# Kernel tuning notes

Hardware: AMD Instinct MI355X
Metric: run time of the kernel (lower is better)

Reference implementation:

```python
import jax, jax.numpy as jnp
import numpy as np

DIM_K = 128
MODEL_DIM = 1024
B, S = 8, 2048

def setup_inputs() -> dict:
    key = jax.random.key(0)
    k1, k2, k3, k4, k5, k6, k7 = jax.random.split(key, 7)
    return {
        "query": jax.random.normal(k1, (B, S, MODEL_DIM), dtype=jnp.float32),
        "key": jax.random.normal(k2, (B, S, MODEL_DIM), dtype=jnp.float32),
        "value": jax.random.normal(k3, (B, S, MODEL_DIM), dtype=jnp.float32),
        "mask": jax.random.randint(k4, (B, S, S), 0, 2, dtype=jnp.int32),
        # nn.Linear(model_dim, dim_k, bias=False): weight shape [dim_k, model_dim]
        "Wq": jax.random.normal(k5, (DIM_K, MODEL_DIM), dtype=jnp.float32) * (MODEL_DIM ** -0.5),
        "Wk": jax.random.normal(k6, (DIM_K, MODEL_DIM), dtype=jnp.float32) * (MODEL_DIM ** -0.5),
        "Wv": jax.random.normal(k7, (DIM_K, MODEL_DIM), dtype=jnp.float32) * (MODEL_DIM ** -0.5),
    }

def reference(query, key, value, mask, Wq, Wk, Wv):
    # projections: y = x @ W.T
    q = jnp.einsum('bsm,km->bsk', query, Wq)
    k = jnp.einsum('bsm,km->bsk', key, Wk)
    v = jnp.einsum('bsm,km->bsk', value, Wv)
    scale = 1.0 / jnp.sqrt(jnp.float32(DIM_K))
    pre_score = jnp.einsum('bqk,bsk->bqs', q, k) * scale  # [B,Sq,Sk]
    pre_score = jnp.where(mask == 0, jnp.float32(-1e9), pre_score)
    score = jax.nn.softmax(pre_score, axis=-1)
    return jnp.einsum('bqs,bsk->bqk', score, v)
```

## Files before the change

kernel.cpp:

```cpp
#include <hip/hip_runtime.h>
#include <hip/hip_fp16.h>

#define SEQ 2048
#define DMODEL 1024
#define DK 128

typedef _Float16 f16x8 __attribute__((ext_vector_type(8)));
typedef float    f32x4 __attribute__((ext_vector_type(4)));

#define L2E 1.44269504088896340736f

#define WS_Q  393216
#define WS_K  2490368
#define WS_VT 4587520
#define WS_F16_BYTES 13369344ull

__global__ __launch_bounds__(256) void wconv_kernel(
    const float* __restrict__ wq, const float* __restrict__ wk,
    const float* __restrict__ wv, _Float16* __restrict__ w16)
{
    int i = blockIdx.x * 256 + threadIdx.x;
    int p = i >> 17;
    int j = i & 131071;
    const float* src = (p == 0) ? wq : ((p == 1) ? wk : wv);
    float f = src[j];
    if (p == 0) f *= 0.08838834764831845f;
    w16[i] = (_Float16)f;
}

__global__ __launch_bounds__(256, 3) void proj_kernel(
    const float* __restrict__ xq, const float* __restrict__ xk,
    const float* __restrict__ xv, const _Float16* __restrict__ w16,
    _Float16* __restrict__ qws, _Float16* __restrict__ kws, _Float16* __restrict__ vtws)
{
    const int p = blockIdx.y;
    const float* __restrict__ x = (p == 0) ? xq : ((p == 1) ? xk : xv);
    const _Float16* __restrict__ w = w16 + p * 131072;

    const int mtile = blockIdx.x;
    const int m0 = mtile << 6;
    const int t = threadIdx.x;
    const int wv_ = t >> 6;
    const int lane = t & 63;
    const int l15 = lane & 15, g = lane >> 4;
    const int mw = m0 + wv_ * 16;

    __shared__ __align__(16) _Float16 smem[18432];

    f32x4 acc[8];
#pragma unroll
    for (int nt = 0; nt < 8; ++nt) acc[nt] = (f32x4){0.f, 0.f, 0.f, 0.f};

    const float* x0 = x + (size_t)(mw + l15) * 1024 + g * 8;
    const int srow = t >> 3, skc = t & 7;
    const _Float16* wsrc = w + (size_t)srow * 1024 + skc * 8;
    const int sdst = srow * 72 + skc * 8;

    f16x8 wreg[2][4];
    f32x4 areg[2][4];

#pragma unroll
    for (int j = 0; j < 4; ++j)
        wreg[0][j] = *(const f16x8*)(wsrc + (size_t)j * 32 * 1024);
#pragma unroll
    for (int s = 0; s < 2; ++s) {
        areg[0][s * 2]     = *(const f32x4*)(x0 + s * 32);
        areg[0][s * 2 + 1] = *(const f32x4*)(x0 + s * 32 + 4);
    }

#pragma unroll
    for (int kt = 0; kt < 16; ++kt) {
        const int c = kt & 1;
        _Float16* buf = smem + c * 9216;

#pragma unroll
        for (int j = 0; j < 4; ++j)
            *(f16x8*)(buf + j * 32 * 72 + sdst) = wreg[c][j];
        __syncthreads();

        if (kt < 15) {
#pragma unroll
            for (int j = 0; j < 4; ++j)
                wreg[c ^ 1][j] = *(const f16x8*)(wsrc + (size_t)j * 32 * 1024
                                                 + (kt + 1) * 64);
#pragma unroll
            for (int s = 0; s < 2; ++s) {
                areg[c ^ 1][s * 2]     = *(const f32x4*)(x0 + (kt + 1) * 64 + s * 32);
                areg[c ^ 1][s * 2 + 1] = *(const f32x4*)(x0 + (kt + 1) * 64 + s * 32 + 4);
            }
        }

#pragma unroll
        for (int s = 0; s < 2; ++s) {
            f16x8 af;
#pragma unroll
            for (int j = 0; j < 4; ++j) {
                af[j]     = (_Float16)areg[c][s * 2][j];
                af[4 + j] = (_Float16)areg[c][s * 2 + 1][j];
            }
#pragma unroll
            for (int nt = 0; nt < 8; ++nt) {
                f16x8 bf = *(const f16x8*)(buf + (nt * 16 + l15) * 72 + s * 32 + g * 8);
                acc[nt] = __builtin_amdgcn_mfma_f32_16x16x32_f16(af, bf, acc[nt], 0, 0, 0);
            }
        }
    }

    __syncthreads();
    _Float16* olds = smem;
#pragma unroll
    for (int nt = 0; nt < 8; ++nt)
#pragma unroll
        for (int r = 0; r < 4; ++r) {
            int rowl = wv_ * 16 + g * 4 + r;
            int col = nt * 16 + l15;
            _Float16 v = (_Float16)acc[nt][r];
            if (p < 2) olds[rowl * 136 + col] = v;
            else       olds[col * 72 + rowl] = v;
        }
    __syncthreads();

    if (p < 2) {
#pragma unroll
        for (int i = 0; i < 4; ++i) {
            int idx = i * 256 + t;
            int row = idx >> 4, ck = idx & 15;
            f16x8 v = *(const f16x8*)(olds + row * 136 + ck * 8);
            _Float16* dst = ((p == 0) ? qws : kws) + (size_t)(m0 + row) * 128 + ck * 8;
            *(f16x8*)dst = v;
        }
    } else {
        const int bq = mtile >> 5, s0 = (mtile & 31) << 6;
#pragma unroll
        for (int i = 0; i < 4; ++i) {
            int idx = i * 256 + t;
            int row = idx >> 3, ck = idx & 7;
            f16x8 v = *(const f16x8*)(olds + row * 72 + ck * 8);
            _Float16* dst = vtws + ((size_t)(bq * 128 + row)) * 2048 + s0 + ck * 8;
            *(f16x8*)dst = v;
        }
    }
}

__global__ __launch_bounds__(256) void flash_kernel(
    const _Float16* __restrict__ qws, const _Float16* __restrict__ kws,
    const _Float16* __restrict__ vtws, const int* __restrict__ mask,
    float* __restrict__ out, float* __restrict__ part, float* __restrict__ mlbuf,
    int ktp)
{
    const int bb = blockIdx.x & 7;
    const int rest = blockIdx.x >> 3;
    const int mtile = rest & 31;
    const int jsplit = rest >> 5;
    const int sq0 = mtile << 6;
    const int t = threadIdx.x;
    const int wv_ = t >> 6;
    const int lane = t & 63;
    const int l15 = lane & 15, g = lane >> 4;

    __shared__ __align__(16) _Float16 smem[22528];
    _Float16* klds = smem;
    _Float16* vtlds = smem + 8704;
    _Float16* plds = smem + 17920 + wv_ * 1152;

    f16x8 qf[4];
    {
        const _Float16* qp = qws + ((size_t)(bb * 2048 + sq0 + wv_ * 16 + l15)) * 128 + g * 8;
#pragma unroll
        for (int ks = 0; ks < 4; ++ks) qf[ks] = *(const f16x8*)(qp + ks * 32);
    }

    f32x4 o[8];
#pragma unroll
    for (int nt = 0; nt < 8; ++nt) o[nt] = (f32x4){0.f, 0.f, 0.f, 0.f};
    float m_run[4], l_run[4];
#pragma unroll
    for (int r = 0; r < 4; ++r) { m_run[r] = -__builtin_inff(); l_run[r] = 0.f; }

    const int* mbase = mask + ((size_t)(bb * 2048 + sq0 + wv_ * 16 + g * 4)) * 2048 + l15;

    const int kt_begin = jsplit * ktp, kt_end = kt_begin + ktp;
    for (int kt = kt_begin; kt < kt_end; ++kt) {
        const int n0 = kt << 6;
        __syncthreads();
#pragma unroll
        for (int i = 0; i < 8; ++i) {
            int idx = i * 256 + t;
            if (idx < 1024) {
                int row = idx >> 4, ck = idx & 15;
                *(f16x8*)(klds + row * 136 + ck * 8) =
                    *(const f16x8*)(kws + ((size_t)(bb * 2048 + n0 + row)) * 128 + ck * 8);
            } else {
                int v = idx - 1024;
                int row = v >> 3, ck = v & 7;
                *(f16x8*)(vtlds + row * 72 + ck * 8) =
                    *(const f16x8*)(vtws + ((size_t)(bb * 128 + row)) * 2048 + n0 + ck * 8);
            }
        }
        __syncthreads();

        int mv[4][4];
#pragma unroll
        for (int nt = 0; nt < 4; ++nt)
#pragma unroll
            for (int r = 0; r < 4; ++r)
                mv[nt][r] = mbase[(size_t)r * 2048 + n0 + nt * 16];

        f32x4 sf[4];
#pragma unroll
        for (int nt = 0; nt < 4; ++nt) sf[nt] = (f32x4){0.f, 0.f, 0.f, 0.f};
#pragma unroll
        for (int nt = 0; nt < 4; ++nt) {
            const _Float16* kp = klds + (nt * 16 + l15) * 136 + g * 8;
#pragma unroll
            for (int ks = 0; ks < 4; ++ks) {
                f16x8 bfk = *(const f16x8*)(kp + ks * 32);
                sf[nt] = __builtin_amdgcn_mfma_f32_16x16x32_f16(qf[ks], bfk, sf[nt], 0, 0, 0);
            }
        }

        float mx[4], mnew[4], alpha[4], psum[4];
#pragma unroll
        for (int r = 0; r < 4; ++r)
            mx[r] = fmaxf(fmaxf(sf[0][r], sf[1][r]), fmaxf(sf[2][r], sf[3][r]));
#pragma unroll
        for (int off = 1; off < 16; off <<= 1)
#pragma unroll
            for (int r = 0; r < 4; ++r)
                mx[r] = fmaxf(mx[r], __shfl_xor(mx[r], off, 64));
#pragma unroll
        for (int r = 0; r < 4; ++r) {
            mnew[r] = fmaxf(m_run[r], mx[r]);
            alpha[r] = exp2f((m_run[r] - mnew[r]) * L2E);
            psum[r] = 0.f;
        }
#pragma unroll
        for (int nt = 0; nt < 4; ++nt)
#pragma unroll
            for (int r = 0; r < 4; ++r) {
                float pv = exp2f((sf[nt][r] - mnew[r]) * L2E);
                pv = mv[nt][r] ? pv : 0.f;
                psum[r] += pv;
                plds[(g * 4 + r) * 72 + nt * 16 + l15] = (_Float16)pv;
            }
#pragma unroll
        for (int off = 1; off < 16; off <<= 1)
#pragma unroll
            for (int r = 0; r < 4; ++r)
                psum[r] += __shfl_xor(psum[r], off, 64);
#pragma unroll
        for (int r = 0; r < 4; ++r) {
            l_run[r] = l_run[r] * alpha[r] + psum[r];
            m_run[r] = mnew[r];
        }
#pragma unroll
        for (int nt = 0; nt < 8; ++nt)
#pragma unroll
            for (int r = 0; r < 4; ++r) o[nt][r] *= alpha[r];

        f16x8 pa[2];
#pragma unroll
        for (int ks2 = 0; ks2 < 2; ++ks2)
            pa[ks2] = *(const f16x8*)(plds + l15 * 72 + ks2 * 32 + g * 8);

#pragma unroll
        for (int nt2 = 0; nt2 < 8; ++nt2) {
            const _Float16* vp = vtlds + (nt2 * 16 + l15) * 72 + g * 8;
#pragma unroll
            for (int ks2 = 0; ks2 < 2; ++ks2) {
                f16x8 bfv = *(const f16x8*)(vp + ks2 * 32);
                o[nt2] = __builtin_amdgcn_mfma_f32_16x16x32_f16(pa[ks2], bfv, o[nt2], 0, 0, 0);
            }
        }
    }

    if (part == nullptr) {
        float inv[4];
#pragma unroll
        for (int r = 0; r < 4; ++r) inv[r] = 1.0f / l_run[r];
#pragma unroll
        for (int nt2 = 0; nt2 < 8; ++nt2)
#pragma unroll
            for (int r = 0; r < 4; ++r)
                out[((size_t)(bb * 2048 + sq0 + wv_ * 16 + g * 4 + r)) * 128 + nt2 * 16 + l15] =
                    o[nt2][r] * inv[r];
    } else {
#pragma unroll
        for (int nt2 = 0; nt2 < 8; ++nt2)
#pragma unroll
            for (int r = 0; r < 4; ++r) {
                size_t rowg = (size_t)(bb * 2048 + sq0 + wv_ * 16 + g * 4 + r);
                part[((size_t)jsplit * 16384 + rowg) * 128 + nt2 * 16 + l15] = o[nt2][r];
            }
        if (l15 == 0) {
#pragma unroll
            for (int r = 0; r < 4; ++r) {
                size_t rowg = (size_t)(bb * 2048 + sq0 + wv_ * 16 + g * 4 + r);
                mlbuf[((size_t)jsplit * 16384 + rowg) * 2]     = m_run[r];
                mlbuf[((size_t)jsplit * 16384 + rowg) * 2 + 1] = l_run[r];
            }
        }
    }
}

__global__ __launch_bounds__(256) void merge_kernel(
    const float* __restrict__ part, const float* __restrict__ mlbuf,
    float* __restrict__ out, int J)
{
    int t = threadIdx.x;
    size_t row = (size_t)blockIdx.x * 8 + (t >> 5);
    int c = (t & 31) * 4;
    float mj[4];
    float m = -__builtin_inff();
    for (int j = 0; j < J; ++j) {
        mj[j] = mlbuf[((size_t)j * 16384 + row) * 2];
        m = fmaxf(m, mj[j]);
    }
    float l = 0.f;
    f32x4 acc = (f32x4){0.f, 0.f, 0.f, 0.f};
    for (int j = 0; j < J; ++j) {
        float w = exp2f((mj[j] - m) * L2E);
        l += w * mlbuf[((size_t)j * 16384 + row) * 2 + 1];
        f32x4 v = *(const f32x4*)(part + ((size_t)j * 16384 + row) * 128 + c);
#pragma unroll
        for (int e = 0; e < 4; ++e) acc[e] += w * v[e];
    }
    float inv = 1.0f / l;
#pragma unroll
    for (int e = 0; e < 4; ++e) acc[e] *= inv;
    *(f32x4*)(out + row * 128 + c) = acc;
}

extern "C" void kernel_launch(void* const* d_in, const int* in_sizes, int n_in,
                              void* d_out, int out_size, void* d_ws, size_t ws_size,
                              hipStream_t stream)
{
    const float* query = (const float*)d_in[0];
    const float* key   = (const float*)d_in[1];
    const float* value = (const float*)d_in[2];
    const int*   mask  = (const int*)d_in[3];
    const float* Wq    = (const float*)d_in[4];
    const float* Wk    = (const float*)d_in[5];
    const float* Wv    = (const float*)d_in[6];
    float* out = (float*)d_out;

    _Float16* w16 = (_Float16*)d_ws;
    _Float16* qws = w16 + WS_Q;
    _Float16* kws = w16 + WS_K;
    _Float16* vtws = w16 + WS_VT;

    const size_t per_split = 16384ull * 128 * 4 + 16384ull * 8;
    int J = 1;
    if (ws_size >= WS_F16_BYTES + 4 * per_split)      J = 4;
    else if (ws_size >= WS_F16_BYTES + 2 * per_split) J = 2;
    float* part = (J > 1) ? (float*)((char*)d_ws + WS_F16_BYTES) : nullptr;
    float* mlbuf = (J > 1) ? (part + (size_t)J * 16384 * 128) : nullptr;

    wconv_kernel<<<1536, 256, 0, stream>>>(Wq, Wk, Wv, w16);
    proj_kernel<<<dim3(256, 3), 256, 0, stream>>>(query, key, value, w16, qws, kws, vtws);
    flash_kernel<<<256 * J, 256, 0, stream>>>(qws, kws, vtws, mask, out, part, mlbuf, 32 / J);
    if (J > 1) merge_kernel<<<2048, 256, 0, stream>>>(part, mlbuf, out, J);
}
```

Baseline: 381.6 us.

## Prefetch K/V/mask tiles into registers, XOR-swizzle LDS, ballot-pack mask bits

The flash kernel now loads the next K, V^T and mask tile into registers while computing the current one, replacing the synchronous global-to-LDS copy at the top of each iteration. Mask values are read with coalesced per-lane loads and packed into 64-bit ballot masks instead of strided scalar reads. LDS padding is replaced by XOR swizzling in both the projection and flash kernels, which shrinks shared memory. The cost is higher register pressure from the staging registers and an extra barrier per k-step in the projection kernel.

```diff
diff --git a/kernel.cpp b/kernel.cpp
--- a/kernel.cpp
+++ b/kernel.cpp
@@ -43,9 +43,10 @@
     const int wv_ = t >> 6;
     const int lane = t & 63;
     const int l15 = lane & 15, g = lane >> 4;
+    const int l7 = lane & 7;
     const int mw = m0 + wv_ * 16;
 
-    __shared__ __align__(16) _Float16 smem[18432];
+    __shared__ __align__(16) _Float16 smem[16384];
 
     f32x4 acc[8];
 #pragma unroll
@@ -54,7 +55,7 @@
     const float* x0 = x + (size_t)(mw + l15) * 1024 + g * 8;
     const int srow = t >> 3, skc = t & 7;
     const _Float16* wsrc = w + (size_t)srow * 1024 + skc * 8;
-    const int sdst = srow * 72 + skc * 8;
+    const int sdst = srow * 64 + ((skc ^ (srow & 7)) << 3);
 
     f16x8 wreg[2][4];
     f32x4 areg[2][4];
@@ -71,11 +72,11 @@
 #pragma unroll
     for (int kt = 0; kt < 16; ++kt) {
         const int c = kt & 1;
-        _Float16* buf = smem + c * 9216;
+        _Float16* buf = smem + c * 8192;
 
 #pragma unroll
         for (int j = 0; j < 4; ++j)
-            *(f16x8*)(buf + j * 32 * 72 + sdst) = wreg[c][j];
+            *(f16x8*)(buf + j * 32 * 64 + sdst) = wreg[c][j];
         __syncthreads();
 
         if (kt < 15) {
@@ -100,13 +101,14 @@
             }
 #pragma unroll
             for (int nt = 0; nt < 8; ++nt) {
-                f16x8 bf = *(const f16x8*)(buf + (nt * 16 + l15) * 72 + s * 32 + g * 8);
+                f16x8 bf = *(const f16x8*)(buf + (nt * 16 + l15) * 64
+                                           + ((((s << 2) | g) ^ l7) << 3));
                 acc[nt] = __builtin_amdgcn_mfma_f32_16x16x32_f16(af, bf, acc[nt], 0, 0, 0);
             }
         }
-    }
-
-    __syncthreads();
+        __syncthreads();
+    }
+
     _Float16* olds = smem;
 #pragma unroll
     for (int nt = 0; nt < 8; ++nt)
@@ -157,11 +159,12 @@
     const int wv_ = t >> 6;
     const int lane = t & 63;
     const int l15 = lane & 15, g = lane >> 4;
-
-    __shared__ __align__(16) _Float16 smem[22528];
+    const int l7 = lane & 7;
+
+    __shared__ __align__(16) _Float16 smem[20480];
     _Float16* klds = smem;
-    _Float16* vtlds = smem + 8704;
-    _Float16* plds = smem + 17920 + wv_ * 1152;
+    _Float16* vtlds = smem + 8192;
+    _Float16* plds = smem + 16384 + wv_ * 1024;
 
     f16x8 qf[4];
     {
@@ -177,44 +180,70 @@
 #pragma unroll
     for (int r = 0; r < 4; ++r) { m_run[r] = -__builtin_inff(); l_run[r] = 0.f; }
 
-    const int* mbase = mask + ((size_t)(bb * 2048 + sq0 + wv_ * 16 + g * 4)) * 2048 + l15;
+    const int* msrc = mask + ((size_t)(bb * 2048 + sq0 + wv_ * 16)) * 2048 + lane;
+
+    const int krow = t >> 4, kck = t & 15;
+    const _Float16* ksrc = kws + ((size_t)(bb * 2048 + krow)) * 128 + kck * 8;
+    _Float16* kdst = klds + krow * 128 + ((kck ^ (krow & 7)) << 3);
+    const int vrow = t >> 3, vck = t & 7;
+    const _Float16* vsrc = vtws + ((size_t)(bb * 128 + vrow)) * 2048 + vck * 8;
+    _Float16* vdst = vtlds + vrow * 64 + ((vck ^ (vrow & 7)) << 3);
+
+    f16x8 kst[4], vst[4];
+    int mint[16];
 
     const int kt_begin = jsplit * ktp, kt_end = kt_begin + ktp;
+
+    {
+        const int n0 = kt_begin << 6;
+#pragma unroll
+        for (int i = 0; i < 4; ++i)
+            kst[i] = *(const f16x8*)(ksrc + (size_t)(n0 + i * 16) * 128);
+#pragma unroll
+        for (int i = 0; i < 4; ++i)
+            vst[i] = *(const f16x8*)(vsrc + (size_t)i * 32 * 2048 + n0);
+#pragma unroll
+        for (int j = 0; j < 16; ++j)
+            mint[j] = msrc[(size_t)j * 2048 + n0];
+    }
+
     for (int kt = kt_begin; kt < kt_end; ++kt) {
-        const int n0 = kt << 6;
         __syncthreads();
 #pragma unroll
-        for (int i = 0; i < 8; ++i) {
-            int idx = i * 256 + t;
-            if (idx < 1024) {
-                int row = idx >> 4, ck = idx & 15;
-                *(f16x8*)(klds + row * 136 + ck * 8) =
-                    *(const f16x8*)(kws + ((size_t)(bb * 2048 + n0 + row)) * 128 + ck * 8);
-            } else {
-                int v = idx - 1024;
-                int row = v >> 3, ck = v & 7;
-                *(f16x8*)(vtlds + row * 72 + ck * 8) =
-                    *(const f16x8*)(vtws + ((size_t)(bb * 128 + row)) * 2048 + n0 + ck * 8);
-            }
-        }
+        for (int i = 0; i < 4; ++i) *(f16x8*)(kdst + i * 16 * 128) = kst[i];
+#pragma unroll
+        for (int i = 0; i < 4; ++i) *(f16x8*)(vdst + i * 32 * 64) = vst[i];
         __syncthreads();
 
-        int mv[4][4];
-#pragma unroll
-        for (int nt = 0; nt < 4; ++nt)
-#pragma unroll
-            for (int r = 0; r < 4; ++r)
-                mv[nt][r] = mbase[(size_t)r * 2048 + n0 + nt * 16];
+        unsigned long long m64[4] = {0ull, 0ull, 0ull, 0ull};
+#pragma unroll
+        for (int j = 0; j < 16; ++j) {
+            unsigned long long b = __ballot(mint[j] != 0);
+            m64[j & 3] = ((j >> 2) == g) ? b : m64[j & 3];
+        }
+
+        if (kt + 1 < kt_end) {
+            const int n1 = (kt + 1) << 6;
+#pragma unroll
+            for (int i = 0; i < 4; ++i)
+                kst[i] = *(const f16x8*)(ksrc + (size_t)(n1 + i * 16) * 128);
+#pragma unroll
+            for (int i = 0; i < 4; ++i)
+                vst[i] = *(const f16x8*)(vsrc + (size_t)i * 32 * 2048 + n1);
+#pragma unroll
+            for (int j = 0; j < 16; ++j)
+                mint[j] = msrc[(size_t)j * 2048 + n1];
+        }
 
         f32x4 sf[4];
 #pragma unroll
         for (int nt = 0; nt < 4; ++nt) sf[nt] = (f32x4){0.f, 0.f, 0.f, 0.f};
 #pragma unroll
         for (int nt = 0; nt < 4; ++nt) {
-            const _Float16* kp = klds + (nt * 16 + l15) * 136 + g * 8;
+            const _Float16* kp = klds + (nt * 16 + l15) * 128;
 #pragma unroll
             for (int ks = 0; ks < 4; ++ks) {
-                f16x8 bfk = *(const f16x8*)(kp + ks * 32);
+                f16x8 bfk = *(const f16x8*)(kp + ((((ks << 2) | g) ^ l7) << 3));
                 sf[nt] = __builtin_amdgcn_mfma_f32_16x16x32_f16(qf[ks], bfk, sf[nt], 0, 0, 0);
             }
         }
@@ -239,9 +268,11 @@
 #pragma unroll
             for (int r = 0; r < 4; ++r) {
                 float pv = exp2f((sf[nt][r] - mnew[r]) * L2E);
-                pv = mv[nt][r] ? pv : 0.f;
+                pv = ((m64[r] >> (nt * 16 + l15)) & 1ull) ? pv : 0.f;
                 psum[r] += pv;
-                plds[(g * 4 + r) * 72 + nt * 16 + l15] = (_Float16)pv;
+                int rr = g * 4 + r;
+                plds[rr * 64 + ((((nt << 1) | (l15 >> 3)) ^ (rr & 7)) << 3) + (l15 & 7)]
+                    = (_Float16)pv;
             }
 #pragma unroll
         for (int off = 1; off < 16; off <<= 1)
@@ -261,14 +292,14 @@
         f16x8 pa[2];
 #pragma unroll
         for (int ks2 = 0; ks2 < 2; ++ks2)
-            pa[ks2] = *(const f16x8*)(plds + l15 * 72 + ks2 * 32 + g * 8);
+            pa[ks2] = *(const f16x8*)(plds + l15 * 64 + ((((ks2 << 2) | g) ^ l7) << 3));
 
 #pragma unroll
         for (int nt2 = 0; nt2 < 8; ++nt2) {
-            const _Float16* vp = vtlds + (nt2 * 16 + l15) * 72 + g * 8;
+            const _Float16* vp = vtlds + (nt2 * 16 + l15) * 64;
 #pragma unroll
             for (int ks2 = 0; ks2 < 2; ++ks2) {
-                f16x8 bfv = *(const f16x8*)(vp + ks2 * 32);
+                f16x8 bfv = *(const f16x8*)(vp + ((((ks2 << 2) | g) ^ l7) << 3));
                 o[nt2] = __builtin_amdgcn_mfma_f32_16x16x32_f16(pa[ks2], bfv, o[nt2], 0, 0, 0);
             }
         }
```

Result: faster. 374.1 us (-2.0%).
